# Kernel optimization log

Measured on AMD Instinct MI355X. Metric: run time of the kernel, lower is better.

## Reference

```python
import jax, jax.numpy as jnp
from jax import lax
import numpy as np

SR = 44100
WAVETABLE_SIZE = 882  # int(SR // freq) for freq = 50 Hz
N_SAMPLES = 8388608


def biquad(x, b0, b1, b2, a0, a1, a2):
    # Direct-form-I biquad, sequential over samples (matches torchaudio biquads).
    b0n, b1n, b2n = b0 / a0, b1 / a0, b2 / a0
    a1n, a2n = a1 / a0, a2 / a0
    z = jnp.zeros((), x.dtype)

    def step(c, xn):
        x1, x2, y1, y2 = c
        yn = b0n * xn + b1n * x1 + b2n * x2 - a1n * y1 - a2n * y2
        return (xn, x1, yn, y1), yn

    _, y = lax.scan(step, (z, z, z, z), x)
    return y


def lowpass_biquad(x, sr, freq, q):
    w0 = 2.0 * jnp.pi * freq / sr
    alpha = jnp.sin(w0) / (2.0 * q)
    cosw = jnp.cos(w0)
    b0 = (1.0 - cosw) / 2.0
    b1 = 1.0 - cosw
    b2 = b0
    return biquad(x, b0, b1, b2, 1.0 + alpha, -2.0 * cosw, 1.0 - alpha)


def bandreject_biquad(x, sr, freq, q):
    w0 = 2.0 * jnp.pi * freq / sr
    alpha = jnp.sin(w0) / (2.0 * q)
    cosw = jnp.cos(w0)
    return biquad(x, 1.0, -2.0 * cosw, 1.0, 1.0 + alpha, -2.0 * cosw, 1.0 - alpha)


def karplus_strong(wavetable, n_samples, decay, feedback_line, feedbackamt):
    # Sequential block-wise Karplus-Strong: feedback inject + distort + roll + decay.
    W = wavetable.shape[0]
    nb = n_samples // W
    cw0 = lax.stop_gradient(wavetable)  # original detaches the wavetable
    blocks = feedback_line[: nb * W].reshape(nb, W)

    def step(cw, fb_block):
        # SoftClipping distortion approximated as tanh soft clip
        cw = cw + jnp.tanh(feedbackamt * fb_block)
        cw = decay * 0.5 * (cw + jnp.roll(cw, 1))
        return cw, cw

    cw, outs = lax.scan(step, cw0, blocks)
    samples = outs.reshape(-1)
    rem = n_samples % W
    if rem > 0:
        cw = decay * 0.5 * (cw + jnp.roll(cw, 1))
        samples = jnp.concatenate([samples, cw[:rem]])
    return samples


def setup_inputs() -> dict:
    key = jax.random.key(0)
    k1, k2, k3, k4, k5 = jax.random.split(key, 5)
    feedback_line = jax.random.normal(k1, (N_SAMPLES,), jnp.float32) * 0.1
    wavetable = 2.0 * jax.random.uniform(k2, (WAVETABLE_SIZE,), jnp.float32) - 1.0
    h = jax.random.uniform(k3, (1, 7), jnp.float32)
    env_params = jax.random.uniform(k4, (3,), jnp.float32)
    lp2_cutoff = jax.random.uniform(k5, (1,), jnp.float32)
    return {"feedback_line": feedback_line, "wavetable": wavetable, "h": h,
            "env_params": env_params, "lp2_cutoff": lp2_cutoff,
            "output_length_samples": N_SAMPLES}


def reference(feedback_line, wavetable, h, env_params, lp2_cutoff, output_length_samples):
    latents = h[:, 0:7]
    decay = jnp.clip(latents[:, 0] / 10.0 + 0.9, 0.9, 0.999)[0]

    lp_freq = jnp.clip(latents[0, 1] * SR / 4.0, 100.0, SR / 2.0 - 1.0)
    lp_q = jnp.clip(latents[0, 2], 0.1, 0.999)
    wt = lowpass_biquad(wavetable, SR, lp_freq, lp_q)
    # LearnableLowpass (init cutoff 8 kHz) modeled as a biquad with learned cutoff
    cutoff2 = 100.0 + lp2_cutoff[0] * 8000.0
    wt = lowpass_biquad(wt, SR, cutoff2, 0.707)

    # NOTE: original computes a clamped feedback_amt but uses the unclamped value.
    feedbackamt = latents[0, 3]
    out = karplus_strong(wt, output_length_samples, decay, feedback_line, feedbackamt)

    fade = jnp.linspace(1.0, 0.0, 256, dtype=out.dtype)
    out = out.at[-256:].multiply(fade)

    br_freq = jnp.clip(latents[0, 5] * SR / 4.0, 100.0, SR / 2.0 - 1.0)
    br_q = jnp.clip(latents[0, 6], 0.1, 0.999)
    out = bandreject_biquad(out, SR, br_freq, br_q)

    # LearnableASR(3): attack / sustain / release envelope (piecewise-linear)
    n = out.shape[0]
    idx = jnp.arange(n, dtype=out.dtype)
    attack = 1.0 + env_params[0] * 0.1 * n
    release = 1.0 + env_params[2] * 0.1 * n
    sustain = jnp.clip(env_params[1], 0.0, 1.0)
    env = jnp.clip(idx / attack, 0.0, 1.0) * jnp.clip((n - 1 - idx) / release, 0.0, 1.0) * sustain
    return out * env * latents[0, 4]
```

## Files before the change

### kernel.cpp

```cpp
#include <hip/hip_runtime.h>
#include <math.h>

#define SRF 44100.0f
#define TWO_PI 6.283185307179586f
#define W 882
#define NHALF 441
#define NFREQ 442
#define MCH 30
#define G_CH 317
#define NS 8388608
#define REMSTART 8387820
#define REMN 788
#define BRL 128
#define BRC 65536
#define WDEPTH 32

#define WS_CH   1024
#define WS_DH   281344
#define WS_CH0  561600
#define WS_BRD  1024
#define WS_BRS  (WS_BRD + 2*BRC)
#define WS_XT1  (WS_BRS + 2*BRC)
#define WS_XT2  (WS_XT1 + BRC)

__device__ __forceinline__ float clipf(float x, float lo, float hi) {
    return fminf(fmaxf(x, lo), hi);
}

__device__ float resolvent(float a1f, float a2f, int n) {
    double a1 = (double)a1f, a2 = (double)a2f;
    double disc = a1*a1 - 4.0*a2;
    double scale = a1*a1 + 4.0*fabs(a2) + 1e-30;
    if (disc > 1e-9*scale) {
        double sq = sqrt(disc);
        double p1 = 0.5*(-a1+sq), p2 = 0.5*(-a1-sq);
        int k = n+1;
        double t1 = pow(fabs(p1), (double)k); if (p1 < 0.0 && (k&1)) t1 = -t1;
        double t2 = pow(fabs(p2), (double)k); if (p2 < 0.0 && (k&1)) t2 = -t2;
        return (float)((t1 - t2)/sq);
    } else if (disc < -1e-9*scale) {
        double r = sqrt(a2);
        double ct = -a1/(2.0*r);
        ct = fmin(1.0, fmax(-1.0, ct));
        double th = acos(ct);
        double sth = sin(th);
        double rn = pow(r, (double)n);
        return (float)(rn * sin((double)(n+1)*th) / sth);
    } else {
        double p = -0.5*a1;
        double t = pow(fabs(p), (double)n); if (p < 0.0 && (n&1)) t = -t;
        return (float)((double)(n+1)*t);
    }
}

__global__ __launch_bounds__(448) void k1_ksA(const float* __restrict__ fb,
                                              const float* __restrict__ wt,
                                              const float* __restrict__ h,
                                              const float* __restrict__ lp2c,
                                              float* __restrict__ ws) {
    __shared__ float sv[W], se[NHALF], so[NHALF];
    __shared__ float sbb[2][8];
    __shared__ float sx[W], sg[W], su[W], sy[W];
    const int t = threadIdx.x;
    const int g = blockIdx.x;

    if (g == G_CH) {
        float b10,b11,b12,a11,a12, b20,b21,b22,a21,a22;
        {
            float freq = clipf(h[1] * (SRF/4.0f), 100.0f, SRF/2.0f - 1.0f);
            float q    = clipf(h[2], 0.1f, 0.999f);
            float w0 = TWO_PI * freq / SRF;
            float sw = sinf(w0), cw = cosf(w0);
            float alpha = sw / (2.0f * q);
            float b0 = (1.0f - cw) * 0.5f, b1 = 1.0f - cw, b2 = b0;
            float a0 = 1.0f + alpha, a1 = -2.0f * cw, a2 = 1.0f - alpha;
            b10=b0/a0; b11=b1/a0; b12=b2/a0; a11=a1/a0; a12=a2/a0;
        }
        {
            float freq = 100.0f + lp2c[0]*8000.0f;
            float q = 0.707f;
            float w0 = TWO_PI * freq / SRF;
            float sw = sinf(w0), cw = cosf(w0);
            float alpha = sw / (2.0f * q);
            float b0 = (1.0f - cw) * 0.5f, b1 = 1.0f - cw, b2 = b0;
            float a0 = 1.0f + alpha, a1 = -2.0f * cw, a2 = 1.0f - alpha;
            b20=b0/a0; b21=b1/a0; b22=b2/a0; a21=a1/a0; a22=a2/a0;
        }
        const int i0 = t, i1 = t + NHALF;
        if (t < NHALF) {
            sx[i0] = wt[i0]; sx[i1] = wt[i1];
            sg[i0] = resolvent(a11, a12, i0);
            sg[i1] = resolvent(a11, a12, i1);
        }
        __syncthreads();
        if (t < NHALF) {
            float acc = 0.0f;
            for (int k = 0; k <= i0; k++) acc += sg[k]*sx[i0-k];
            su[i0] = acc;
            acc = 0.0f;
            for (int k = 0; k <= i1; k++) acc += sg[k]*sx[i1-k];
            su[i1] = acc;
        }
        __syncthreads();
        if (t < NHALF) {
            float y = b10*su[i0];
            if (i0 >= 1) y += b11*su[i0-1];
            if (i0 >= 2) y += b12*su[i0-2];
            sy[i0] = y;
            y = b20*su[i1-0]*0.0f;
            y = b10*su[i1] + b11*su[i1-1] + b12*su[i1-2];
            sy[i1] = y;
            sg[i0] = resolvent(a21, a22, i0);
            sg[i1] = resolvent(a21, a22, i1);
        }
        __syncthreads();
        if (t < NHALF) {
            float acc = 0.0f;
            for (int k = 0; k <= i0; k++) acc += sg[k]*sy[i0-k];
            su[i0] = acc;
            acc = 0.0f;
            for (int k = 0; k <= i1; k++) acc += sg[k]*sy[i1-k];
            su[i1] = acc;
        }
        __syncthreads();
        if (t < NHALF) {
            float y = b20*su[i0];
            if (i0 >= 1) y += b21*su[i0-1];
            if (i0 >= 2) y += b22*su[i0-2];
            sv[i0] = y;
            y = b20*su[i1] + b21*su[i1-1] + b22*su[i1-2];
            sv[i1] = y;
        }
        __syncthreads();
        if (t < NHALF) { se[t] = sv[t] + sv[t+NHALF]; so[t] = sv[t] - sv[t+NHALF]; }
        __syncthreads();
        if (t < NFREQ) {
            const int f = t;
            const float* yb = (f & 1) ? so : se;
            float ang = (float)f * (TWO_PI / (float)W);
            float S, C; __sincosf(ang, &S, &C);
            float cr = 1.0f, ci = 0.0f;
            float re = 0.0f, im = 0.0f;
            for (int k = 0; k < NHALF; k++) {
                float y = yb[k];
                re = fmaf(y, cr, re);
                im = fmaf(y, ci, im);
                float tt = cr;
                cr = fmaf(tt, C,  ci*S);
                ci = fmaf(ci, C, -tt*S);
            }
            ws[WS_CH0 + 2*f]   = re;
            ws[WS_CH0 + 2*f+1] = im;
        }
        return;
    }

    const float decay = clipf(h[0] / 10.0f + 0.9f, 0.9f, 0.999f);
    const float d2 = decay * 0.5f;
    const float fa = h[3];
    const int lane = t & 63, wv = t >> 6;
    const bool act = (t < NHALF);
    const float* fbp2 = fb + (long)g*MCH*W + 2*t;
    float z0 = 0.0f, z1 = 0.0f;
    float2 cur = act ? *(const float2*)fbp2 : make_float2(0.f,0.f);
    for (int j = 0; j < MCH; j++) {
        float2 nxt = make_float2(0.f,0.f);
        if (j+1 < MCH && act) nxt = *(const float2*)(fbp2 + (long)(j+1)*W);
        float v0 = z0 + tanhf(fa*cur.x);
        float v1 = z1 + tanhf(fa*cur.y);
        if (lane == 63 && wv < 6) sbb[j&1][wv+1] = v1;
        if (t == NHALF-1)         sbb[j&1][0]    = v1;
        float vs = __shfl_up(v1, 1);
        __syncthreads();
        float vp = (lane == 0) ? sbb[j&1][wv] : vs;
        z0 = d2*(v0 + vp);
        z1 = d2*(v1 + v0);
        cur = nxt;
    }
    if (act) { sv[2*t] = z0; sv[2*t+1] = z1; }
    __syncthreads();
    if (t < NHALF) { se[t] = sv[t] + sv[t+NHALF]; so[t] = sv[t] - sv[t+NHALF]; }
    __syncthreads();
    if (t < NFREQ) {
        const int f = t;
        const float* yb = (f & 1) ? so : se;
        float ang = (float)f * (TWO_PI / (float)W);
        float S, C; __sincosf(ang, &S, &C);
        float cr = 1.0f, ci = 0.0f;
        float re = 0.0f, im = 0.0f;
        for (int k = 0; k < NHALF; k++) {
            float y = yb[k];
            re = fmaf(y, cr, re);
            im = fmaf(y, ci, im);
            float tt = cr;
            cr = fmaf(tt, C,  ci*S);
            ci = fmaf(ci, C, -tt*S);
        }
        float* dst = ws + WS_DH + (long)g*(2*NFREQ);
        dst[2*f]   = re;
        dst[2*f+1] = im;
    }
}

__global__ __launch_bounds__(64) void kB_scan(const float* __restrict__ h,
                                              float* __restrict__ ws) {
    const int f = blockIdx.x*64 + threadIdx.x;
    if (f >= NFREQ) return;
    const float decay = clipf(h[0] / 10.0f + 0.9f, 0.9f, 0.999f);
    const float d2 = decay * 0.5f;
    double phi = (double)f * (double)(TWO_PI) / (double)W;
    double m2 = 2.0 * (double)d2 * cos(0.5*phi);
    double mag = pow(m2, (double)MCH);
    double ang = -0.5 * (double)MCH * phi;
    float mre = (float)(mag * cos(ang));
    float mim = (float)(mag * sin(ang));
    float cre = ws[WS_CH0 + 2*f];
    float cim = ws[WS_CH0 + 2*f+1];
    float* CH = ws + WS_CH;
    const float* DH = ws + WS_DH;
    CH[2*f] = cre; CH[2*f+1] = cim;
    float cr8[8], ci8[8], nr8[8], ni8[8];
    #pragma unroll
    for (int u = 0; u < 8; u++) {
        cr8[u] = DH[(long)u*(2*NFREQ) + 2*f];
        ci8[u] = DH[(long)u*(2*NFREQ) + 2*f+1];
    }
    for (int b = 0; b < 39; b++) {
        const int gnext = 1 + (b+1)*8;
        if (b < 38) {
            #pragma unroll
            for (int u = 0; u < 8; u++) {
                nr8[u] = DH[(long)(gnext-1+u)*(2*NFREQ) + 2*f];
                ni8[u] = DH[(long)(gnext-1+u)*(2*NFREQ) + 2*f+1];
            }
        } else {
            #pragma unroll
            for (int u = 0; u < 4; u++) {
                nr8[u] = DH[(long)(gnext-1+u)*(2*NFREQ) + 2*f];
                ni8[u] = DH[(long)(gnext-1+u)*(2*NFREQ) + 2*f+1];
            }
        }
        const int g0 = 1 + b*8;
        #pragma unroll
        for (int u = 0; u < 8; u++) {
            float nre = mre*cre - mim*cim + cr8[u];
            float nim = mre*cim + mim*cre + ci8[u];
            cre = nre; cim = nim;
            CH[(long)(g0+u)*(2*NFREQ) + 2*f]   = cre;
            CH[(long)(g0+u)*(2*NFREQ) + 2*f+1] = cim;
        }
        #pragma unroll
        for (int u = 0; u < 8; u++) { cr8[u] = nr8[u]; ci8[u] = ni8[u]; }
    }
    #pragma unroll
    for (int u = 0; u < 4; u++) {
        float nre = mre*cre - mim*cim + cr8[u];
        float nim = mre*cim + mim*cre + ci8[u];
        cre = nre; cim = nim;
        CH[(long)(313+u)*(2*NFREQ) + 2*f]   = cre;
        CH[(long)(313+u)*(2*NFREQ) + 2*f+1] = cim;
    }
}

__global__ __launch_bounds__(448) void k3_ksC(const float* __restrict__ fb,
                                              const float* __restrict__ h,
                                              const float* __restrict__ ws,
                                              float* __restrict__ out) {
    __shared__ float chs[2*NFREQ];
    __shared__ float cini[W];
    __shared__ float sbb[2][8];
    const int t = threadIdx.x;
    const int lane = t & 63, wv = t >> 6;
    const int g = blockIdx.x;
    const float decay = clipf(h[0] / 10.0f + 0.9f, 0.9f, 0.999f);
    const float d2 = decay * 0.5f;
    const float fa = h[3];
    const bool act = (t < NHALF);
    {
        const float* src = ws + WS_CH + (long)g*(2*NFREQ);
        if (t < NFREQ) { chs[2*t] = src[2*t]; chs[2*t+1] = src[2*t+1]; }
    }
    __syncthreads();
    if (act) {
        const int j = t;
        float aj = (float)j * (TWO_PI / (float)W);
        float sA, cA; __sincosf(aj, &sA, &cA);
        float s2, c2; __sincosf(2.0f*aj, &s2, &c2);
        float rr = 1.0f, ri = 0.0f;
        float RE = 0.0f, SOr = 0.0f, SOi = 0.0f;
        for (int m = 0; m < 220; m++) {
            float xr = chs[4*m+2], xi = chs[4*m+3];
            SOr = fmaf(xr, rr, SOr); SOr = fmaf(-xi, ri, SOr);
            SOi = fmaf(xr, ri, SOi); SOi = fmaf( xi, rr, SOi);
            float tr = rr;
            rr = fmaf(tr, c2, -ri*s2);
            ri = fmaf(ri, c2,  tr*s2);
            float yr = chs[4*m+4], yi = chs[4*m+5];
            RE = fmaf(yr, rr, RE); RE = fmaf(-yi, ri, RE);
        }
        float RO = cA*SOr - sA*SOi;
        float sgn = (j & 1) ? -1.0f : 1.0f;
        float base0 = chs[0] + sgn*chs[2*NHALF];
        float base1 = chs[0] - sgn*chs[2*NHALF];
        cini[j]        = (base0 + 2.0f*(RE + RO)) * (1.0f/(float)W);
        cini[j+NHALF]  = (base1 + 2.0f*(RE - RO)) * (1.0f/(float)W);
    }
    __syncthreads();
    float z0 = act ? cini[2*t]   : 0.0f;
    float z1 = act ? cini[2*t+1] : 0.0f;
    const float* fbp2 = fb + (long)g*MCH*W + 2*t;
    float* outp2 = out + (long)g*MCH*W + 2*t;
    float2 cur = act ? *(const float2*)fbp2 : make_float2(0.f,0.f);
    for (int j = 0; j < MCH; j++) {
        float2 nxt = make_float2(0.f,0.f);
        if (j+1 < MCH && act) nxt = *(const float2*)(fbp2 + (long)(j+1)*W);
        float v0 = z0 + tanhf(fa*cur.x);
        float v1 = z1 + tanhf(fa*cur.y);
        if (lane == 63 && wv < 6) sbb[j&1][wv+1] = v1;
        if (t == NHALF-1)         sbb[j&1][0]    = v1;
        float vs = __shfl_up(v1, 1);
        __syncthreads();
        float vp = (lane == 0) ? sbb[j&1][wv] : vs;
        z0 = d2*(v0 + vp);
        z1 = d2*(v1 + v0);
        if (act) *(float2*)(outp2 + (long)j*W) = make_float2(z0, z1);
        cur = nxt;
    }
    if (g == G_CH-1) {
        float v0 = z0, v1 = z1;
        if (lane == 63 && wv < 6) sbb[0][wv+1] = v1;
        if (t == NHALF-1)         sbb[0][0]    = v1;
        float vs = __shfl_up(v1, 1);
        __syncthreads();
        float vp = (lane == 0) ? sbb[0][wv] : vs;
        float r0 = d2*(v0 + vp);
        float r1 = d2*(v1 + v0);
        if (t < REMN/2) {
            int idx0 = REMSTART + 2*t;
            int idx1 = idx0 + 1;
            if (idx0 >= NS-256) r0 *= (1.0f - (float)(idx0-(NS-256))*(1.0f/255.0f));
            if (idx1 >= NS-256) r1 *= (1.0f - (float)(idx1-(NS-256))*(1.0f/255.0f));
            *(float2*)(out + idx0) = make_float2(r0, r1);
        }
    }
}

__global__ __launch_bounds__(256) void k4_br1(const float* __restrict__ x,
                                              const float* __restrict__ h,
                                              float* __restrict__ ws) {
    __shared__ float tile[256*33];
    const int tid = threadIdx.x;
    const int c = blockIdx.x*256 + tid;
    const long base = (long)blockIdx.x * (256*BRL);
    float B0,B1,B2,A1,A2;
    {
        float freq = clipf(h[5]*(SRF/4.0f), 100.0f, SRF/2.0f - 1.0f);
        float q = clipf(h[6], 0.1f, 0.999f);
        float w0 = TWO_PI * freq / SRF;
        float sw = sinf(w0), cw = cosf(w0);
        float alpha = sw / (2.0f * q);
        float a0 = 1.0f + alpha;
        B0 = 1.0f/a0; B1 = (-2.0f*cw)/a0; B2 = 1.0f/a0;
        A1 = (-2.0f*cw)/a0; A2 = (1.0f - alpha)/a0;
    }
    float x1, x2, y1=0.f, y2=0.f;
    {
        long g0 = (long)c * BRL;
        x1 = (c>0) ? x[g0-1] : 0.0f;
        x2 = (c>0) ? x[g0-2] : 0.0f;
    }
    for (int tt=0; tt<BRL/32; tt++) {
        const float4* src4 = (const float4*)(x + base + (long)tt*32);
        for (int q = tid; q < 256*8; q += 256) {
            int r = q >> 3, c4 = q & 7;
            float4 v = src4[(long)r*(BRL/4) + c4];
            tile[r*33 + c4*4 + 0] = v.x;
            tile[r*33 + c4*4 + 1] = v.y;
            tile[r*33 + c4*4 + 2] = v.z;
            tile[r*33 + c4*4 + 3] = v.w;
        }
        __syncthreads();
        #pragma unroll
        for (int j=0;j<32;j++){
            float xv = tile[tid*33 + j];
            float y = B0*xv + B1*x1 + B2*x2 - A1*y1 - A2*y2;
            x2=x1; x1=xv; y2=y1; y1=y;
        }
        __syncthreads();
    }
    ws[WS_BRD + 2*c]   = y1;
    ws[WS_BRD + 2*c+1] = y2;
    ws[WS_XT1 + c] = x1;
    ws[WS_XT2 + c] = x2;
}

__global__ __launch_bounds__(256) void kP_state(const float* __restrict__ h,
                                                float* __restrict__ ws) {
    __shared__ float sld[2*(256+WDEPTH)];
    const int tid = threadIdx.x;
    const int bid = blockIdx.x;
    float A1,A2;
    {
        float freq = clipf(h[5]*(SRF/4.0f), 100.0f, SRF/2.0f - 1.0f);
        float q = clipf(h[6], 0.1f, 0.999f);
        float w0 = TWO_PI * freq / SRF;
        float sw = sinf(w0), cw = cosf(w0);
        float alpha = sw / (2.0f * q);
        float a0 = 1.0f + alpha;
        A1 = (-2.0f*cw)/a0; A2 = (1.0f - alpha)/a0;
    }
    double t00=-A1, t01=-A2, t10=1.0, t11=0.0;
    for (int k=0;k<7;k++){
        double na=t00*t00+t01*t10, nb=t00*t01+t01*t11;
        double nc=t10*t00+t11*t10, nd=t10*t01+t11*t11;
        t00=na;t01=nb;t10=nc;t11=nd;
    }
    const float T00=(float)t00, T01=(float)t01, T10=(float)t10, T11=(float)t11;
    const int base = bid*256 - WDEPTH;
    for (int j = tid; j < 256+WDEPTH; j += 256) {
        int r = base + j;
        float a=0.f, b=0.f;
        if (r >= 0) { a = ws[WS_BRD + 2*r]; b = ws[WS_BRD + 2*r + 1]; }
        sld[2*j] = a; sld[2*j+1] = b;
    }
    __syncthreads();
    const int li = tid + WDEPTH;
    float e1 = sld[2*(li-1)], e2 = sld[2*(li-1)+1];
    float P00=T00,P01=T01,P10=T10,P11=T11;
    #pragma unroll 4
    for (int u = 1; u < WDEPTH; u++) {
        float d1 = sld[2*(li-1-u)], d2_ = sld[2*(li-1-u)+1];
        e1 = fmaf(P00,d1, fmaf(P01,d2_, e1));
        e2 = fmaf(P10,d1, fmaf(P11,d2_, e2));
        float n00 = P00*T00+P01*T10, n01 = P00*T01+P01*T11;
        float n10 = P10*T00+P11*T10, n11 = P10*T01+P11*T11;
        P00=n00;P01=n01;P10=n10;P11=n11;
    }
    const int c = bid*256 + tid;
    ws[WS_BRS + 2*c]   = e1;
    ws[WS_BRS + 2*c+1] = e2;
}

__global__ __launch_bounds__(256) void k6_br2(float* __restrict__ x,
                                              const float* __restrict__ h,
                                              const float* __restrict__ envp,
                                              const float* __restrict__ ws) {
    __shared__ float tile[256*33];
    const int tid = threadIdx.x;
    const int c = blockIdx.x*256 + tid;
    const long base = (long)blockIdx.x * (256*BRL);
    float B0,B1,B2,A1,A2;
    {
        float freq = clipf(h[5]*(SRF/4.0f), 100.0f, SRF/2.0f - 1.0f);
        float q = clipf(h[6], 0.1f, 0.999f);
        float w0 = TWO_PI * freq / SRF;
        float sw = sinf(w0), cw = cosf(w0);
        float alpha = sw / (2.0f * q);
        float a0 = 1.0f + alpha;
        B0 = 1.0f/a0; B1 = (-2.0f*cw)/a0; B2 = 1.0f/a0;
        A1 = (-2.0f*cw)/a0; A2 = (1.0f - alpha)/a0;
    }
    const float nF = (float)NS;
    const float invA = 1.0f/(1.0f + envp[0]*0.1f*nF);
    const float invR = 1.0f/(1.0f + envp[2]*0.1f*nF);
    const float sa_ = clipf(envp[1], 0.0f, 1.0f) * h[4];
    float x1 = (c>0)? ws[WS_XT1 + c-1] : 0.0f;
    float x2 = (c>0)? ws[WS_XT2 + c-1] : 0.0f;
    float y1 = ws[WS_BRS + 2*c];
    float y2 = ws[WS_BRS + 2*c+1];
    for (int tt=0; tt<BRL/32; tt++) {
        float4* dst4 = (float4*)(x + base + (long)tt*32);
        for (int q = tid; q < 256*8; q += 256) {
            int r = q >> 3, c4 = q & 7;
            float4 v = ((const float4*)dst4)[(long)r*(BRL/4) + c4];
            tile[r*33 + c4*4 + 0] = v.x;
            tile[r*33 + c4*4 + 1] = v.y;
            tile[r*33 + c4*4 + 2] = v.z;
            tile[r*33 + c4*4 + 3] = v.w;
        }
        __syncthreads();
        #pragma unroll
        for (int j=0;j<32;j++){
            float xv = tile[tid*33 + j];
            float y = B0*xv + B1*x1 + B2*x2 - A1*y1 - A2*y2;
            x2=x1; x1=xv; y2=y1; y1=y;
            int idx = c*BRL + tt*32 + j;
            float ea = fminf((float)idx * invA, 1.0f);
            float er = fminf((float)(NS-1-idx) * invR, 1.0f);
            tile[tid*33 + j] = y * (ea*er*sa_);
        }
        __syncthreads();
        for (int q = tid; q < 256*8; q += 256) {
            int r = q >> 3, c4 = q & 7;
            float4 v;
            v.x = tile[r*33 + c4*4 + 0];
            v.y = tile[r*33 + c4*4 + 1];
            v.z = tile[r*33 + c4*4 + 2];
            v.w = tile[r*33 + c4*4 + 3];
            dst4[(long)r*(BRL/4) + c4] = v;
        }
        __syncthreads();
    }
}

extern "C" void kernel_launch(void* const* d_in, const int* in_sizes, int n_in,
                              void* d_out, int out_size, void* d_ws, size_t ws_size,
                              hipStream_t stream) {
    const float* fb   = (const float*)d_in[0];
    const float* wt   = (const float*)d_in[1];
    const float* h    = (const float*)d_in[2];
    const float* envp = (const float*)d_in[3];
    const float* lp2c = (const float*)d_in[4];
    float* out = (float*)d_out;
    float* ws  = (float*)d_ws;

    hipLaunchKernelGGL(k1_ksA,   dim3(G_CH+1), dim3(448), 0, stream, fb, wt, h, lp2c, ws);
    hipLaunchKernelGGL(kB_scan,  dim3(7),      dim3(64),  0, stream, h, ws);
    hipLaunchKernelGGL(k3_ksC,   dim3(G_CH),   dim3(448), 0, stream, fb, h, ws, out);
    hipLaunchKernelGGL(k4_br1,   dim3(256),    dim3(256), 0, stream, out, h, ws);
    hipLaunchKernelGGL(kP_state, dim3(256),    dim3(256), 0, stream, h, ws);
    hipLaunchKernelGGL(k6_br2,   dim3(256),    dim3(256), 0, stream, out, h, envp, ws);
}
```

Before: 231.5 us.

## Replace per-step block barriers in Karplus-Strong scans with wave-local halo recompute

Result: faster. 218.1 us (-5.8%).

```diff
diff --git a/kernel.cpp b/kernel.cpp
--- a/kernel.cpp
+++ b/kernel.cpp
@@ -14,6 +14,9 @@
 #define BRL 128
 #define BRC 65536
 #define WDEPTH 32
+#define HALO 31
+#define OWNW 126
+#define NPOS 157
 
 #define WS_CH   1024
 #define WS_DH   281344
@@ -53,14 +56,15 @@
     }
 }
 
-__global__ __launch_bounds__(448) void k1_ksA(const float* __restrict__ fb,
+__global__ __launch_bounds__(448) void kD_ksA(const float* __restrict__ fb,
                                               const float* __restrict__ wt,
                                               const float* __restrict__ h,
                                               const float* __restrict__ lp2c,
                                               float* __restrict__ ws) {
-    __shared__ float sv[W], se[NHALF], so[NHALF];
-    __shared__ float sbb[2][8];
-    __shared__ float sx[W], sg[W], su[W], sy[W];
+    __shared__ float sv[W];
+    __shared__ __align__(16) float se[444];
+    __shared__ __align__(16) float so[444];
+    __shared__ float sx[W], sg[W], su[W], sy2[W];
     const int t = threadIdx.x;
     const int g = blockIdx.x;
 
@@ -86,119 +90,97 @@
             float a0 = 1.0f + alpha, a1 = -2.0f * cw, a2 = 1.0f - alpha;
             b20=b0/a0; b21=b1/a0; b22=b2/a0; a21=a1/a0; a22=a2/a0;
         }
-        const int i0 = t, i1 = t + NHALF;
+        const int i0 = t, i1 = W-1-t;
         if (t < NHALF) {
-            sx[i0] = wt[i0]; sx[i1] = wt[i1];
-            sg[i0] = resolvent(a11, a12, i0);
-            sg[i1] = resolvent(a11, a12, i1);
+            sx[i0]=wt[i0]; sx[i1]=wt[i1];
+            sg[i0]=resolvent(a11,a12,i0); sg[i1]=resolvent(a11,a12,i1);
         }
         __syncthreads();
         if (t < NHALF) {
-            float acc = 0.0f;
-            for (int k = 0; k <= i0; k++) acc += sg[k]*sx[i0-k];
-            su[i0] = acc;
-            acc = 0.0f;
-            for (int k = 0; k <= i1; k++) acc += sg[k]*sx[i1-k];
-            su[i1] = acc;
+            float acc=0.f; for (int k=0;k<=i0;k++) acc += sg[k]*sx[i0-k]; su[i0]=acc;
+            acc=0.f;       for (int k=0;k<=i1;k++) acc += sg[k]*sx[i1-k]; su[i1]=acc;
         }
         __syncthreads();
         if (t < NHALF) {
-            float y = b10*su[i0];
-            if (i0 >= 1) y += b11*su[i0-1];
-            if (i0 >= 2) y += b12*su[i0-2];
-            sy[i0] = y;
-            y = b20*su[i1-0]*0.0f;
+            float y = b10*su[i0]; if (i0>=1) y+=b11*su[i0-1]; if (i0>=2) y+=b12*su[i0-2];
+            sy2[i0]=y;
             y = b10*su[i1] + b11*su[i1-1] + b12*su[i1-2];
-            sy[i1] = y;
-            sg[i0] = resolvent(a21, a22, i0);
-            sg[i1] = resolvent(a21, a22, i1);
-        }
+            sy2[i1]=y;
+        }
+        __syncthreads();
+        if (t < NHALF) { sg[i0]=resolvent(a21,a22,i0); sg[i1]=resolvent(a21,a22,i1); }
         __syncthreads();
         if (t < NHALF) {
-            float acc = 0.0f;
-            for (int k = 0; k <= i0; k++) acc += sg[k]*sy[i0-k];
-            su[i0] = acc;
-            acc = 0.0f;
-            for (int k = 0; k <= i1; k++) acc += sg[k]*sy[i1-k];
-            su[i1] = acc;
+            float acc=0.f; for (int k=0;k<=i0;k++) acc += sg[k]*sy2[i0-k]; su[i0]=acc;
+            acc=0.f;       for (int k=0;k<=i1;k++) acc += sg[k]*sy2[i1-k]; su[i1]=acc;
         }
         __syncthreads();
         if (t < NHALF) {
-            float y = b20*su[i0];
-            if (i0 >= 1) y += b21*su[i0-1];
-            if (i0 >= 2) y += b22*su[i0-2];
-            sv[i0] = y;
+            float y = b20*su[i0]; if (i0>=1) y+=b21*su[i0-1]; if (i0>=2) y+=b22*su[i0-2];
+            sv[i0]=y;
             y = b20*su[i1] + b21*su[i1-1] + b22*su[i1-2];
-            sv[i1] = y;
-        }
-        __syncthreads();
-        if (t < NHALF) { se[t] = sv[t] + sv[t+NHALF]; so[t] = sv[t] - sv[t+NHALF]; }
-        __syncthreads();
-        if (t < NFREQ) {
-            const int f = t;
-            const float* yb = (f & 1) ? so : se;
-            float ang = (float)f * (TWO_PI / (float)W);
-            float S, C; __sincosf(ang, &S, &C);
-            float cr = 1.0f, ci = 0.0f;
-            float re = 0.0f, im = 0.0f;
-            for (int k = 0; k < NHALF; k++) {
-                float y = yb[k];
-                re = fmaf(y, cr, re);
-                im = fmaf(y, ci, im);
-                float tt = cr;
-                cr = fmaf(tt, C,  ci*S);
-                ci = fmaf(ci, C, -tt*S);
-            }
-            ws[WS_CH0 + 2*f]   = re;
-            ws[WS_CH0 + 2*f+1] = im;
-        }
-        return;
-    }
-
-    const float decay = clipf(h[0] / 10.0f + 0.9f, 0.9f, 0.999f);
-    const float d2 = decay * 0.5f;
-    const float fa = h[3];
-    const int lane = t & 63, wv = t >> 6;
-    const bool act = (t < NHALF);
-    const float* fbp2 = fb + (long)g*MCH*W + 2*t;
-    float z0 = 0.0f, z1 = 0.0f;
-    float2 cur = act ? *(const float2*)fbp2 : make_float2(0.f,0.f);
-    for (int j = 0; j < MCH; j++) {
-        float2 nxt = make_float2(0.f,0.f);
-        if (j+1 < MCH && act) nxt = *(const float2*)(fbp2 + (long)(j+1)*W);
-        float v0 = z0 + tanhf(fa*cur.x);
-        float v1 = z1 + tanhf(fa*cur.y);
-        if (lane == 63 && wv < 6) sbb[j&1][wv+1] = v1;
-        if (t == NHALF-1)         sbb[j&1][0]    = v1;
-        float vs = __shfl_up(v1, 1);
-        __syncthreads();
-        float vp = (lane == 0) ? sbb[j&1][wv] : vs;
-        z0 = d2*(v0 + vp);
-        z1 = d2*(v1 + v0);
-        cur = nxt;
-    }
-    if (act) { sv[2*t] = z0; sv[2*t+1] = z1; }
+            sv[i1]=y;
+        }
+    } else {
+        const float decay = clipf(h[0]/10.0f + 0.9f, 0.9f, 0.999f);
+        const float d2 = decay*0.5f;
+        const float fa = h[3];
+        const int lane = t & 63, wv = t >> 6;
+        const int q0 = 3*lane;
+        const int bp = OWNW*wv - HALO;
+        const bool va0 = (q0   < NPOS), va1 = (q0+1 < NPOS), va2 = (q0+2 < NPOS);
+        int p0 = bp + q0, p1 = p0+1, p2 = p0+2;
+        int pw0 = va0 ? (p0<0 ? p0+W : p0) : 0;
+        int pw1 = va1 ? (p1<0 ? p1+W : p1) : 0;
+        int pw2 = va2 ? (p2<0 ? p2+W : p2) : 0;
+        const float* fbg = fb + (long)g*(MCH*W);
+        float z0=0.f, z1=0.f, z2=0.f;
+        float c0 = fbg[pw0], c1 = fbg[pw1], c2v = fbg[pw2];
+        for (int j=0;j<MCH;j++){
+            float n0=0.f,n1=0.f,n2=0.f;
+            if (j+1<MCH){ const float* fj = fbg + (j+1)*W; n0=fj[pw0]; n1=fj[pw1]; n2=fj[pw2]; }
+            float v0 = z0 + tanhf(fa*c0);
+            float v1 = z1 + tanhf(fa*c1);
+            float v2 = z2 + tanhf(fa*c2v);
+            float vp = __shfl_up(v2, 1);
+            z0 = d2*(v0+vp); z1 = d2*(v1+v0); z2 = d2*(v2+v1);
+            c0=n0; c1=n1; c2v=n2;
+        }
+        if (va0 && q0   >= HALO) sv[p0] = z0;
+        if (va1 && q0+1 >= HALO) sv[p1] = z1;
+        if (va2 && q0+2 >= HALO) sv[p2] = z2;
+    }
     __syncthreads();
-    if (t < NHALF) { se[t] = sv[t] + sv[t+NHALF]; so[t] = sv[t] - sv[t+NHALF]; }
+    if (t < NHALF) { se[t] = sv[t]+sv[t+NHALF]; so[t] = sv[t]-sv[t+NHALF]; }
     __syncthreads();
     if (t < NFREQ) {
         const int f = t;
+        const float phf = (float)f * (TWO_PI/(float)W);
+        float s1v, c1v; __sincosf(phf, &s1v, &c1v);
+        float s4v, c4v; __sincosf(4.0f*phf, &s4v, &c4v);
         const float* yb = (f & 1) ? so : se;
-        float ang = (float)f * (TWO_PI / (float)W);
-        float S, C; __sincosf(ang, &S, &C);
-        float cr = 1.0f, ci = 0.0f;
-        float re = 0.0f, im = 0.0f;
-        for (int k = 0; k < NHALF; k++) {
-            float y = yb[k];
-            re = fmaf(y, cr, re);
-            im = fmaf(y, ci, im);
-            float tt = cr;
-            cr = fmaf(tt, C,  ci*S);
-            ci = fmaf(ci, C, -tt*S);
-        }
-        float* dst = ws + WS_DH + (long)g*(2*NFREQ);
-        dst[2*f]   = re;
-        dst[2*f+1] = im;
+        float a0r=0.f,a0i=0.f,a1r=0.f,a1i=0.f,a2r=0.f,a2i=0.f,a3r=0.f,a3i=0.f;
+        float rr=1.0f, ri=0.0f;
+        for (int m=0;m<110;m++){
+            float4 y = *((const float4*)yb + m);
+            a0r = fmaf(y.x, rr, a0r); a0i = fmaf(y.x, ri, a0i);
+            a1r = fmaf(y.y, rr, a1r); a1i = fmaf(y.y, ri, a1i);
+            a2r = fmaf(y.z, rr, a2r); a2i = fmaf(y.z, ri, a2i);
+            a3r = fmaf(y.w, rr, a3r); a3i = fmaf(y.w, ri, a3i);
+            float tr = rr;
+            rr = fmaf(tr, c4v,  ri*s4v);
+            ri = fmaf(ri, c4v, -tr*s4v);
+        }
+        a0r = fmaf(yb[440], rr, a0r); a0i = fmaf(yb[440], ri, a0i);
+        float w1r = c1v,  w1i = -s1v;
+        float w2r = c1v*c1v - s1v*s1v;
+        float w2i = -2.0f*c1v*s1v;
+        float w3r = w1r*w2r - w1i*w2i;
+        float w3i = w1r*w2i + w1i*w2r;
+        float Xr = a0r + w1r*a1r - w1i*a1i + w2r*a2r - w2i*a2i + w3r*a3r - w3i*a3i;
+        float Xi = a0i + w1r*a1i + w1i*a1r + w2r*a2i + w2i*a2r + w3r*a3i + w3i*a3r;
+        float2* dst = (float2*)(ws + ((g==G_CH) ? (long)WS_CH0 : (long)WS_DH + (long)g*(2*NFREQ)));
+        dst[f] = make_float2(Xr, Xi);
     }
 }
 
@@ -268,20 +250,17 @@
                                               float* __restrict__ out) {
     __shared__ float chs[2*NFREQ];
     __shared__ float cini[W];
-    __shared__ float sbb[2][8];
     const int t = threadIdx.x;
-    const int lane = t & 63, wv = t >> 6;
     const int g = blockIdx.x;
-    const float decay = clipf(h[0] / 10.0f + 0.9f, 0.9f, 0.999f);
-    const float d2 = decay * 0.5f;
+    const float decay = clipf(h[0]/10.0f + 0.9f, 0.9f, 0.999f);
+    const float d2 = decay*0.5f;
     const float fa = h[3];
-    const bool act = (t < NHALF);
-    {
-        const float* src = ws + WS_CH + (long)g*(2*NFREQ);
-        if (t < NFREQ) { chs[2*t] = src[2*t]; chs[2*t+1] = src[2*t+1]; }
+    if (t < NFREQ) {
+        float2 v = ((const float2*)(ws + WS_CH + (long)g*(2*NFREQ)))[t];
+        chs[2*t] = v.x; chs[2*t+1] = v.y;
     }
     __syncthreads();
-    if (act) {
+    if (t < NHALF) {
         const int j = t;
         float aj = (float)j * (TWO_PI / (float)W);
         float sA, cA; __sincosf(aj, &sA, &cA);
@@ -306,41 +285,53 @@
         cini[j+NHALF]  = (base1 + 2.0f*(RE - RO)) * (1.0f/(float)W);
     }
     __syncthreads();
-    float z0 = act ? cini[2*t]   : 0.0f;
-    float z1 = act ? cini[2*t+1] : 0.0f;
-    const float* fbp2 = fb + (long)g*MCH*W + 2*t;
-    float* outp2 = out + (long)g*MCH*W + 2*t;
-    float2 cur = act ? *(const float2*)fbp2 : make_float2(0.f,0.f);
-    for (int j = 0; j < MCH; j++) {
-        float2 nxt = make_float2(0.f,0.f);
-        if (j+1 < MCH && act) nxt = *(const float2*)(fbp2 + (long)(j+1)*W);
-        float v0 = z0 + tanhf(fa*cur.x);
-        float v1 = z1 + tanhf(fa*cur.y);
-        if (lane == 63 && wv < 6) sbb[j&1][wv+1] = v1;
-        if (t == NHALF-1)         sbb[j&1][0]    = v1;
-        float vs = __shfl_up(v1, 1);
-        __syncthreads();
-        float vp = (lane == 0) ? sbb[j&1][wv] : vs;
-        z0 = d2*(v0 + vp);
-        z1 = d2*(v1 + v0);
-        if (act) *(float2*)(outp2 + (long)j*W) = make_float2(z0, z1);
-        cur = nxt;
+    const int lane = t & 63, wv = t >> 6;
+    const int q0 = 3*lane;
+    const int bp = OWNW*wv - HALO;
+    const bool va0 = (q0   < NPOS), va1 = (q0+1 < NPOS), va2 = (q0+2 < NPOS);
+    int p0 = bp + q0, p1 = p0+1, p2 = p0+2;
+    int pw0 = va0 ? (p0<0 ? p0+W : p0) : 0;
+    int pw1 = va1 ? (p1<0 ? p1+W : p1) : 0;
+    int pw2 = va2 ? (p2<0 ? p2+W : p2) : 0;
+    const bool ow0 = va0 && q0   >= HALO;
+    const bool ow1 = va1 && q0+1 >= HALO;
+    const bool ow2 = va2 && q0+2 >= HALO;
+    float z0 = cini[pw0], z1 = cini[pw1], z2 = cini[pw2];
+    const float* fbg = fb + (long)g*(MCH*W);
+    float* outg = out + (long)g*(MCH*W);
+    float c0 = fbg[pw0], c1 = fbg[pw1], c2v = fbg[pw2];
+    for (int j=0;j<MCH;j++){
+        float n0=0.f,n1=0.f,n2=0.f;
+        if (j+1<MCH){ const float* fj = fbg + (j+1)*W; n0=fj[pw0]; n1=fj[pw1]; n2=fj[pw2]; }
+        float v0 = z0 + tanhf(fa*c0);
+        float v1 = z1 + tanhf(fa*c1);
+        float v2 = z2 + tanhf(fa*c2v);
+        float vp = __shfl_up(v2, 1);
+        z0 = d2*(v0+vp); z1 = d2*(v1+v0); z2 = d2*(v2+v1);
+        float* oj = outg + (long)j*W;
+        if (ow0) oj[p0] = z0;
+        if (ow1) oj[p1] = z1;
+        if (ow2) oj[p2] = z2;
+        c0=n0; c1=n1; c2v=n2;
     }
     if (g == G_CH-1) {
-        float v0 = z0, v1 = z1;
-        if (lane == 63 && wv < 6) sbb[0][wv+1] = v1;
-        if (t == NHALF-1)         sbb[0][0]    = v1;
-        float vs = __shfl_up(v1, 1);
-        __syncthreads();
-        float vp = (lane == 0) ? sbb[0][wv] : vs;
-        float r0 = d2*(v0 + vp);
-        float r1 = d2*(v1 + v0);
-        if (t < REMN/2) {
-            int idx0 = REMSTART + 2*t;
-            int idx1 = idx0 + 1;
-            if (idx0 >= NS-256) r0 *= (1.0f - (float)(idx0-(NS-256))*(1.0f/255.0f));
-            if (idx1 >= NS-256) r1 *= (1.0f - (float)(idx1-(NS-256))*(1.0f/255.0f));
-            *(float2*)(out + idx0) = make_float2(r0, r1);
+        float v0 = z0, v1 = z1, v2 = z2;
+        float vp = __shfl_up(v2, 1);
+        float r0 = d2*(v0+vp), r1 = d2*(v1+v0), r2 = d2*(v2+v1);
+        if (ow0 && p0 < REMN) {
+            int idx = REMSTART + p0; float r = r0;
+            if (idx >= NS-256) r *= (1.0f - (float)(idx-(NS-256))*(1.0f/255.0f));
+            out[idx] = r;
+        }
+        if (ow1 && p1 < REMN) {
+            int idx = REMSTART + p1; float r = r1;
+            if (idx >= NS-256) r *= (1.0f - (float)(idx-(NS-256))*(1.0f/255.0f));
+            out[idx] = r;
+        }
+        if (ow2 && p2 < REMN) {
+            int idx = REMSTART + p2; float r = r2;
+            if (idx >= NS-256) r *= (1.0f - (float)(idx-(NS-256))*(1.0f/255.0f));
+            out[idx] = r;
         }
     }
 }
@@ -514,7 +505,7 @@
     float* out = (float*)d_out;
     float* ws  = (float*)d_ws;
 
-    hipLaunchKernelGGL(k1_ksA,   dim3(G_CH+1), dim3(448), 0, stream, fb, wt, h, lp2c, ws);
+    hipLaunchKernelGGL(kD_ksA,   dim3(G_CH+1), dim3(448), 0, stream, fb, wt, h, lp2c, ws);
     hipLaunchKernelGGL(kB_scan,  dim3(7),      dim3(64),  0, stream, h, ws);
     hipLaunchKernelGGL(k3_ksC,   dim3(G_CH),   dim3(448), 0, stream, fb, h, ws, out);
     hipLaunchKernelGGL(k4_br1,   dim3(256),    dim3(256), 0, stream, out, h, ws);
```
